# Kernel optimization log

Measured on AMD Instinct MI355X. Metric: run time of the kernel, lower is better.

## Reference

```python
import jax, jax.numpy as jnp
import numpy as np

B, C3, T = 32, 384, 2048

def setup_inputs() -> dict:
    key = jax.random.key(0)
    qkv = jax.random.normal(key, (B, C3, T), dtype=jnp.float32)
    return {"qkv": qkv}

def reference(qkv):
    # qkv: [B, 3C, T]
    ch = qkv.shape[1] // 3
    q, k, v = jnp.split(qkv, 3, axis=1)  # each [B, C, T]
    scale = 1.0 / jnp.sqrt(jnp.asarray(ch, dtype=qkv.dtype))
    # weight[b, t_q, t_k] = sum_c q[b,c,t_q] * k[b,c,t_k]
    weight = jnp.einsum('bcq,bck->bqk', q, k) * scale  # [B, T, T]
    weight = jax.nn.softmax(weight, axis=-1)
    # out[b, c, t_q] = sum_k weight[b,t_q,k] * v[b,c,k]
    out = jnp.einsum('bqk,bck->bcq', weight, v)  # [B, C, T]
    return out
```

## Files before the change

### kernel.cpp

```cpp
#include <hip/hip_runtime.h>
#include <hip/hip_bf16.h>
#include <math.h>

#define BB 32
#define CC 128
#define TT 2048
#define NCH 384

typedef __attribute__((ext_vector_type(8))) short short8;
typedef __attribute__((ext_vector_type(16))) float floatx16;

__device__ ushort g_q[(size_t)BB * TT * CC];
__device__ ushort g_k[(size_t)BB * TT * CC];
__device__ ushort g_v[(size_t)BB * CC * TT];

__device__ __forceinline__ ushort f2bf(float f) {
    uint u = __float_as_uint(f);
    u += 0x7fffu + ((u >> 16) & 1u);
    return (ushort)(u >> 16);
}

typedef __attribute__((address_space(1))) const unsigned char ga_t;
typedef __attribute__((address_space(3))) unsigned char la_t;
__device__ __forceinline__ void glds16(const void* g, void* l) {
    __builtin_amdgcn_global_load_lds((ga_t*)g, (la_t*)l, 16, 0, 0);
}

__global__ __launch_bounds__(256) void prepass_kernel(const float* __restrict__ qkv) {
    __shared__ float lds[64][133];
    const int b = blockIdx.y;
    const int t0 = blockIdx.x * 64;
    const int tid = threadIdx.x;
    const int u = tid >> 3;
    const int j = tid & 7;

    for (int part = 0; part < 2; ++part) {
        const float scale = (part == 0) ? 0.127517451f : 1.0f;
        float4 fa[4][2];
#pragma unroll
        for (int i = 0; i < 4; i++) {
            const float* src = qkv + ((size_t)(b * NCH + part * CC + i * 32 + u)) * TT + t0 + j * 8;
            fa[i][0] = *(const float4*)src;
            fa[i][1] = *(const float4*)(src + 4);
        }
        if (part) __syncthreads();
#pragma unroll
        for (int i = 0; i < 4; i++) {
            int c = i * 32 + u;
#pragma unroll
            for (int q = 0; q < 2; q++) {
                lds[j * 8 + q * 4 + 0][c] = fa[i][q].x;
                lds[j * 8 + q * 4 + 1][c] = fa[i][q].y;
                lds[j * 8 + q * 4 + 2][c] = fa[i][q].z;
                lds[j * 8 + q * 4 + 3][c] = fa[i][q].w;
            }
        }
        __syncthreads();
        ushort* dst = (part == 0 ? g_q : g_k) + ((size_t)(b * TT + t0)) * CC;
#pragma unroll
        for (int p = 0; p < 4; p++) {
            int t = p * 16 + (tid >> 4);
            int x = tid & 15;
            int cb = x ^ (t & 15);
            ushort tmp[8];
#pragma unroll
            for (int jj = 0; jj < 8; jj++) tmp[jj] = f2bf(lds[t][cb * 8 + jj] * scale);
            *(uint4*)(dst + (size_t)t * CC + x * 8) = *(uint4*)tmp;
        }
    }
    {
        const float* vsrc = qkv + ((size_t)(b * NCH + 2 * CC)) * TT + t0;
        ushort* vdst = g_v + ((size_t)(b * CC)) * TT + t0;
#pragma unroll
        for (int i = 0; i < 4; i++) {
            int idx = i * 256 + tid;
            int c = idx >> 3, db = idx & 7, sb = db ^ (c & 7);
            const float* s = vsrc + (size_t)c * TT + sb * 8;
            float4 f0 = *(const float4*)s;
            float4 f1 = *(const float4*)(s + 4);
            ushort tmp[8] = {f2bf(f0.x), f2bf(f0.y), f2bf(f0.z), f2bf(f0.w),
                             f2bf(f1.x), f2bf(f1.y), f2bf(f1.z), f2bf(f1.w)};
            *(uint4*)(vdst + (size_t)c * TT + db * 8) = *(uint4*)tmp;
        }
    }
}

__global__ __launch_bounds__(256) void attn_kernel(float* __restrict__ out) {
    __shared__ ushort smem[32768];

    const int b = blockIdx.y;
    const int q0 = blockIdx.x * 128;
    const int tid = threadIdx.x;
    const int w = tid >> 6;
    const int l = tid & 63;
    const int l31 = l & 31;
    const int hi = l >> 5;
    const int qrow = w * 32 + l31;

    const ushort* gq = g_q + ((size_t)(b * TT + q0)) * CC;
    const ushort* gk = g_k + ((size_t)b * TT) * CC;
    const ushort* gv = g_v + ((size_t)b * CC) * TT;

#pragma unroll
    for (int j = 0; j < 8; j++) {
        int inst = 8 * w + j;
        const ushort* src = gq + (size_t)(4 * inst + (l >> 4)) * CC + (l & 15) * 8;
        glds16(src, smem + 16384 + inst * 512 + l * 8);
    }
    auto stage_kv = [&](int bufoff, int kt0) {
#pragma unroll
        for (int j = 0; j < 4; j++) {
            int inst = 4 * w + j;
            const ushort* src = gk + (size_t)(kt0 + 4 * inst + (l >> 4)) * CC + (l & 15) * 8;
            glds16(src, smem + bufoff + inst * 512 + l * 8);
        }
#pragma unroll
        for (int j = 0; j < 4; j++) {
            int inst = 4 * w + j;
            const ushort* src = gv + (size_t)(8 * inst + (l >> 3)) * TT + kt0 + (l & 7) * 8;
            glds16(src, smem + bufoff + 8192 + inst * 512 + l * 8);
        }
    };
    stage_kv(0, 0);
    __syncthreads();

    short8 qf[8];
#pragma unroll
    for (int ck = 0; ck < 8; ck++) {
        int x = (2 * ck + hi) ^ (qrow & 15);
        qf[ck] = *(const short8*)(smem + 16384 + qrow * 128 + x * 8);
    }
    __syncthreads();

    floatx16 oacc[4];
#pragma unroll
    for (int cm = 0; cm < 4; cm++)
#pragma unroll
        for (int r = 0; r < 16; r++) oacc[cm][r] = 0.f;
    float m_run = -INFINITY;
    float l_run = 0.f;

    auto compute = [&](int bufoff) {
        const ushort* Ksb = smem + bufoff;
        const ushort* Vsb = smem + bufoff + 8192;

        floatx16 sacc[2];
#pragma unroll
        for (int th = 0; th < 2; th++)
#pragma unroll
            for (int r = 0; r < 16; r++) sacc[th][r] = 0.f;
#pragma unroll
        for (int ck = 0; ck < 8; ck++)
#pragma unroll
            for (int th = 0; th < 2; th++) {
                int kt = 32 * th + l31;
                int x = (2 * ck + hi) ^ (kt & 15);
                short8 ak = *(const short8*)(Ksb + kt * 128 + x * 8);
                sacc[th] = __builtin_amdgcn_mfma_f32_32x32x16_bf16(ak, qf[ck], sacc[th], 0, 0, 0);
            }

        float vmax = -INFINITY;
#pragma unroll
        for (int th = 0; th < 2; th++)
#pragma unroll
            for (int r = 0; r < 16; r++) vmax = fmaxf(vmax, sacc[th][r]);
        vmax = fmaxf(vmax, __shfl_xor(vmax, 32));
        if (!__all(vmax <= m_run + 8.0f)) {
            float mnew = fmaxf(m_run, vmax);
            float alpha = exp2f(m_run - mnew);
            l_run *= alpha;
#pragma unroll
            for (int cm = 0; cm < 4; cm++) oacc[cm] = oacc[cm] * alpha;
            m_run = mnew;
        }
        float rs = 0.f;
#pragma unroll
        for (int th = 0; th < 2; th++)
#pragma unroll
            for (int r = 0; r < 16; r++) {
                sacc[th][r] = exp2f(sacc[th][r] - m_run);
                rs += sacc[th][r];
            }
        rs += __shfl_xor(rs, 32);
        l_run += rs;

        uint own[2][8], xch[2][8];
#pragma unroll
        for (int th = 0; th < 2; th++)
#pragma unroll
            for (int q8 = 0; q8 < 8; q8++) {
                __hip_bfloat162 h = __float22bfloat162_rn(
                    make_float2(sacc[th][2 * q8], sacc[th][2 * q8 + 1]));
                own[th][q8] = *(uint*)&h;
                xch[th][q8] = __shfl_xor(own[th][q8], 32);
            }

#pragma unroll
        for (int kbg = 0; kbg < 4; kbg++) {
            int th = kbg >> 1, kb = kbg & 1;
            union { uint u[4]; short8 s; } bu;
            bu.u[0] = hi ? xch[th][4 * kb + 2] : own[th][4 * kb + 0];
            bu.u[1] = hi ? xch[th][4 * kb + 3] : own[th][4 * kb + 1];
            bu.u[2] = hi ? own[th][4 * kb + 2] : xch[th][4 * kb + 0];
            bu.u[3] = hi ? own[th][4 * kb + 3] : xch[th][4 * kb + 1];
#pragma unroll
            for (int cm = 0; cm < 4; cm++) {
                int c = 32 * cm + l31;
                int pos = (2 * kbg + hi) ^ (c & 7);
                short8 av = *(const short8*)(Vsb + c * 64 + pos * 8);
                oacc[cm] = __builtin_amdgcn_mfma_f32_32x32x16_bf16(av, bu.s, oacc[cm], 0, 0, 0);
            }
        }
    };

#pragma unroll 1
    for (int t = 0; t < 32; t += 2) {
        if (t + 1 < 32) stage_kv(16384, (t + 1) * 64);
        compute(0);
        __syncthreads();
        if (t + 2 < 32) stage_kv(0, (t + 2) * 64);
        compute(16384);
        __syncthreads();
    }

    float inv = 1.0f / l_run;
    float* op = out + ((size_t)b * CC) * TT + q0 + w * 32 + l31;
#pragma unroll
    for (int cm = 0; cm < 4; cm++)
#pragma unroll
        for (int r = 0; r < 16; r++) {
            int c = 32 * cm + (r & 3) + 8 * (r >> 2) + 4 * hi;
            op[(size_t)c * TT] = oacc[cm][r] * inv;
        }
}

extern "C" void kernel_launch(void* const* d_in, const int* in_sizes, int n_in,
                              void* d_out, int out_size, void* d_ws, size_t ws_size,
                              hipStream_t stream) {
    (void)in_sizes; (void)n_in; (void)d_ws; (void)ws_size; (void)out_size;
    const float* qkv = (const float*)d_in[0];
    float* out = (float*)d_out;
    hipLaunchKernelGGL(prepass_kernel, dim3(32, 32), dim3(256), 0, stream, qkv);
    hipLaunchKernelGGL(attn_kernel, dim3(16, 32), dim3(256), 0, stream, out);
}
```

Baseline: 291.1 us.

## Halve KV tile to 32 keys to cut LDS and raise attention occupancy

The attention kernel now stages 32-key K/V tiles instead of 64, which halves shared memory to 32KB, and sets launch bounds to allow three blocks per CU. Q fragments are loaded straight from global memory into registers instead of going through LDS, and the V pre-pass swizzle changes to match the narrower 32-column V tile layout. The double-buffer schedule is reordered so the next tile is prefetched right after each barrier. In exchange the loop runs twice as many iterations, so there are more barriers, more online-softmax rescale checks and less work per sync. The register cap from the launch bounds may also cause spills.

```diff
diff --git a/kernel.cpp b/kernel.cpp
--- a/kernel.cpp
+++ b/kernel.cpp
@@ -74,7 +74,8 @@
 #pragma unroll
         for (int i = 0; i < 4; i++) {
             int idx = i * 256 + tid;
-            int c = idx >> 3, db = idx & 7, sb = db ^ (c & 7);
+            int c = idx >> 3, db = idx & 7;
+            int sb = (db & 4) | ((db ^ c) & 3);
             const float* s = vsrc + (size_t)c * TT + sb * 8;
             float4 f0 = *(const float4*)s;
             float4 f1 = *(const float4*)(s + 4);
@@ -85,8 +86,8 @@
     }
 }
 
-__global__ __launch_bounds__(256) void attn_kernel(float* __restrict__ out) {
-    __shared__ ushort smem[32768];
+__global__ __launch_bounds__(256, 3) void attn_kernel(float* __restrict__ out) {
+    __shared__ ushort smem[16384];
 
     const int b = blockIdx.y;
     const int q0 = blockIdx.x * 128;
@@ -101,35 +102,29 @@
     const ushort* gk = g_k + ((size_t)b * TT) * CC;
     const ushort* gv = g_v + ((size_t)b * CC) * TT;
 
-#pragma unroll
-    for (int j = 0; j < 8; j++) {
-        int inst = 8 * w + j;
-        const ushort* src = gq + (size_t)(4 * inst + (l >> 4)) * CC + (l & 15) * 8;
-        glds16(src, smem + 16384 + inst * 512 + l * 8);
-    }
-    auto stage_kv = [&](int bufoff, int kt0) {
-#pragma unroll
-        for (int j = 0; j < 4; j++) {
-            int inst = 4 * w + j;
+    short8 qf[8];
+#pragma unroll
+    for (int ck = 0; ck < 8; ck++) {
+        int x = (2 * ck + hi) ^ (qrow & 15);
+        qf[ck] = *(const short8*)(gq + (size_t)qrow * CC + x * 8);
+    }
+
+    auto stage_kv = [&](int off, int kt0) {
+#pragma unroll
+        for (int j = 0; j < 2; j++) {
+            int inst = 2 * w + j;
             const ushort* src = gk + (size_t)(kt0 + 4 * inst + (l >> 4)) * CC + (l & 15) * 8;
-            glds16(src, smem + bufoff + inst * 512 + l * 8);
-        }
-#pragma unroll
-        for (int j = 0; j < 4; j++) {
-            int inst = 4 * w + j;
-            const ushort* src = gv + (size_t)(8 * inst + (l >> 3)) * TT + kt0 + (l & 7) * 8;
-            glds16(src, smem + bufoff + 8192 + inst * 512 + l * 8);
+            glds16(src, smem + off + inst * 512 + l * 8);
+        }
+#pragma unroll
+        for (int j = 0; j < 2; j++) {
+            int inst = 2 * w + j;
+            const ushort* src = gv + (size_t)(16 * inst + (l >> 2)) * TT + kt0 + (l & 3) * 8;
+            glds16(src, smem + off + 4096 + inst * 512 + l * 8);
         }
     };
     stage_kv(0, 0);
-    __syncthreads();
-
-    short8 qf[8];
-#pragma unroll
-    for (int ck = 0; ck < 8; ck++) {
-        int x = (2 * ck + hi) ^ (qrow & 15);
-        qf[ck] = *(const short8*)(smem + 16384 + qrow * 128 + x * 8);
-    }
+    stage_kv(8192, 32);
     __syncthreads();
 
     floatx16 oacc[4];
@@ -140,30 +135,23 @@
     float m_run = -INFINITY;
     float l_run = 0.f;
 
-    auto compute = [&](int bufoff) {
-        const ushort* Ksb = smem + bufoff;
-        const ushort* Vsb = smem + bufoff + 8192;
-
-        floatx16 sacc[2];
-#pragma unroll
-        for (int th = 0; th < 2; th++)
-#pragma unroll
-            for (int r = 0; r < 16; r++) sacc[th][r] = 0.f;
-#pragma unroll
-        for (int ck = 0; ck < 8; ck++)
-#pragma unroll
-            for (int th = 0; th < 2; th++) {
-                int kt = 32 * th + l31;
-                int x = (2 * ck + hi) ^ (kt & 15);
-                short8 ak = *(const short8*)(Ksb + kt * 128 + x * 8);
-                sacc[th] = __builtin_amdgcn_mfma_f32_32x32x16_bf16(ak, qf[ck], sacc[th], 0, 0, 0);
-            }
+    auto compute = [&](int off) {
+        const ushort* Ksb = smem + off;
+        const ushort* Vsb = smem + off + 4096;
+
+        floatx16 sacc;
+#pragma unroll
+        for (int r = 0; r < 16; r++) sacc[r] = 0.f;
+#pragma unroll
+        for (int ck = 0; ck < 8; ck++) {
+            int x = (2 * ck + hi) ^ (l31 & 15);
+            short8 ak = *(const short8*)(Ksb + l31 * 128 + x * 8);
+            sacc = __builtin_amdgcn_mfma_f32_32x32x16_bf16(ak, qf[ck], sacc, 0, 0, 0);
+        }
 
         float vmax = -INFINITY;
 #pragma unroll
-        for (int th = 0; th < 2; th++)
-#pragma unroll
-            for (int r = 0; r < 16; r++) vmax = fmaxf(vmax, sacc[th][r]);
+        for (int r = 0; r < 16; r++) vmax = fmaxf(vmax, sacc[r]);
         vmax = fmaxf(vmax, __shfl_xor(vmax, 32));
         if (!__all(vmax <= m_run + 8.0f)) {
             float mnew = fmaxf(m_run, vmax);
@@ -175,56 +163,51 @@
         }
         float rs = 0.f;
 #pragma unroll
-        for (int th = 0; th < 2; th++)
-#pragma unroll
-            for (int r = 0; r < 16; r++) {
-                sacc[th][r] = exp2f(sacc[th][r] - m_run);
-                rs += sacc[th][r];
-            }
+        for (int r = 0; r < 16; r++) {
+            sacc[r] = exp2f(sacc[r] - m_run);
+            rs += sacc[r];
+        }
         rs += __shfl_xor(rs, 32);
         l_run += rs;
 
-        uint own[2][8], xch[2][8];
-#pragma unroll
-        for (int th = 0; th < 2; th++)
-#pragma unroll
-            for (int q8 = 0; q8 < 8; q8++) {
-                __hip_bfloat162 h = __float22bfloat162_rn(
-                    make_float2(sacc[th][2 * q8], sacc[th][2 * q8 + 1]));
-                own[th][q8] = *(uint*)&h;
-                xch[th][q8] = __shfl_xor(own[th][q8], 32);
-            }
-
-#pragma unroll
-        for (int kbg = 0; kbg < 4; kbg++) {
-            int th = kbg >> 1, kb = kbg & 1;
+        uint own[8], xch[8];
+#pragma unroll
+        for (int q8 = 0; q8 < 8; q8++) {
+            __hip_bfloat162 h = __float22bfloat162_rn(
+                make_float2(sacc[2 * q8], sacc[2 * q8 + 1]));
+            own[q8] = *(uint*)&h;
+            xch[q8] = __shfl_xor(own[q8], 32);
+        }
+
+#pragma unroll
+        for (int kb = 0; kb < 2; kb++) {
             union { uint u[4]; short8 s; } bu;
-            bu.u[0] = hi ? xch[th][4 * kb + 2] : own[th][4 * kb + 0];
-            bu.u[1] = hi ? xch[th][4 * kb + 3] : own[th][4 * kb + 1];
-            bu.u[2] = hi ? own[th][4 * kb + 2] : xch[th][4 * kb + 0];
-            bu.u[3] = hi ? own[th][4 * kb + 3] : xch[th][4 * kb + 1];
+            bu.u[0] = hi ? xch[4 * kb + 2] : own[4 * kb + 0];
+            bu.u[1] = hi ? xch[4 * kb + 3] : own[4 * kb + 1];
+            bu.u[2] = hi ? own[4 * kb + 2] : xch[4 * kb + 0];
+            bu.u[3] = hi ? own[4 * kb + 3] : xch[4 * kb + 1];
 #pragma unroll
             for (int cm = 0; cm < 4; cm++) {
                 int c = 32 * cm + l31;
-                int pos = (2 * kbg + hi) ^ (c & 7);
-                short8 av = *(const short8*)(Vsb + c * 64 + pos * 8);
+                int pos = (2 * kb + hi) ^ (c & 3);
+                short8 av = *(const short8*)(Vsb + c * 32 + pos * 8);
                 oacc[cm] = __builtin_amdgcn_mfma_f32_32x32x16_bf16(av, bu.s, oacc[cm], 0, 0, 0);
             }
         }
     };
 
 #pragma unroll 1
-    for (int t = 0; t < 32; t += 2) {
-        if (t + 1 < 32) stage_kv(16384, (t + 1) * 64);
+    for (int t = 0; t < 64; t += 2) {
         compute(0);
         __syncthreads();
-        if (t + 2 < 32) stage_kv(0, (t + 2) * 64);
-        compute(16384);
+        if (t + 2 < 64) stage_kv(0, (t + 2) * 32);
+        compute(8192);
         __syncthreads();
+        if (t + 3 < 64) stage_kv(8192, (t + 3) * 32);
     }
 
     float inv = 1.0f / l_run;
-    float* op = out + ((size_t)b * CC) * TT + q0 + w * 32 + l31;
+    float* op = out + ((size_t)b * CC) * TT + q0 + qrow;
 #pragma unroll
     for (int cm = 0; cm < 4; cm++)
 #pragma unroll
```

Result: faster. 265.0 us (-9.0%).
